# Kernel tuning notes

Measured on AMD Instinct MI355X. Metric: run time of the kernel, lower is better.

Reference implementation:

```python
import jax, jax.numpy as jnp
import numpy as np
from jax import lax

B, C_G, H, W = 2, 64, 240, 1216
NUM, K, IDX_REF = 8, 9, 4  # prop_kernel=3
PROP_TIME = 6


def conv3x3(x, w, b):
    y = lax.conv_general_dilated(x, w, (1, 1), ((1, 1), (1, 1)),
                                 dimension_numbers=('NCHW', 'OIHW', 'NCHW'))
    return y + b[None, :, None, None]


def bilinear_sample(img, y, x):
    """img: (B,H,W); y,x: (B,K,H,W) absolute coords; zero padding outside."""
    Hh, Ww = img.shape[1], img.shape[2]
    y0 = jnp.floor(y)
    x0 = jnp.floor(x)
    wy1, wx1 = y - y0, x - x0
    gather = jax.vmap(lambda im, a, b: im[a, b])
    out = jnp.zeros_like(y)
    for i, (yy, wy) in enumerate(((y0, 1.0 - wy1), (y0 + 1.0, wy1))):
        for j, (xx, wx) in enumerate(((x0, 1.0 - wx1), (x0 + 1.0, wx1))):
            valid = (yy >= 0) & (yy <= Hh - 1) & (xx >= 0) & (xx <= Ww - 1)
            yi = jnp.clip(yy, 0, Hh - 1).astype(jnp.int32)
            xi = jnp.clip(xx, 0, Ww - 1).astype(jnp.int32)
            v = gather(img, yi, xi)
            out = out + wy * wx * jnp.where(valid, v, 0.0)
    return out


def setup_inputs() -> dict:
    key = jax.random.key(0)
    ks = jax.random.split(key, 6)
    return {
        'initial_disp': jax.random.uniform(ks[0], (B, 1, H, W), jnp.float32) * 50.0,
        'occlus_mask': jax.random.uniform(ks[1], (B, 1, H, W), jnp.float32),
        'confidence': jax.random.uniform(ks[2], (B, 1, H, W), jnp.float32),
        'guidance_feature': jax.random.normal(ks[3], (B, C_G, H, W), jnp.float32),
        'conv_w': 0.05 * jax.random.normal(ks[4], (3 * NUM, C_G, 3, 3), jnp.float32),
        'conv_b': jnp.zeros((3 * NUM,), jnp.float32),
        'aff_scale_const': jnp.full((1,), 0.5 * NUM, jnp.float32),  # TGASS: gamma*num
    }


def nlspn_forward(initial_disp, occlus_mask, confidence, guidance_feature,
                  conv_w, conv_b, aff_scale_const):
    Bb, _, Hh, Ww = guidance_feature.shape
    oa = conv3x3(guidance_feature, conv_w, conv_b)          # (B, 3*num, H, W)
    o1, o2, aff = oa[:, :NUM], oa[:, NUM:2 * NUM], oa[:, 2 * NUM:]
    off = jnp.concatenate([o1, o2], axis=1).reshape(Bb, NUM, 2, Hh, Ww)
    zero = jnp.zeros((Bb, 1, 2, Hh, Ww), off.dtype)
    off = jnp.concatenate([off[:, :IDX_REF], zero, off[:, IDX_REF:]], axis=1)  # (B,9,2,H,W)

    # TGASS affinity
    aff = jnp.tanh(aff) / (aff_scale_const[0] + 1e-8)       # (B,8,H,W)

    gy = jnp.arange(Hh, dtype=jnp.float32)[None, None, :, None]
    gx = jnp.arange(Ww, dtype=jnp.float32)[None, None, None, :]

    # confidence sampling: 1x1 deform conv (w_conf=1, bias=0), detached offsets
    off_sg = lax.stop_gradient(off)
    nb = jnp.array([0, 1, 2, 3, 5, 6, 7, 8])
    conf_s = bilinear_sample(confidence[:, 0],
                             gy + off_sg[:, nb, 0], gx + off_sg[:, nb, 1])  # (B,8,H,W)
    aff = aff * conf_s

    s = jnp.sum(jnp.abs(aff), axis=1, keepdims=True) + 1e-5
    s = jnp.where(s < 1.0, 1.0, s)
    aff = aff / s
    aff_ref = 1.0 - jnp.sum(aff, axis=1, keepdims=True)
    aff_full = jnp.concatenate([aff[:, :IDX_REF], aff_ref, aff[:, IDX_REF:]], axis=1)  # (B,9,H,W)

    # 3x3 deform conv grid (stride 1, pad 1, dil 1), weight=ones, bias=0
    kh = (jnp.arange(K) // 3 - 1).astype(jnp.float32).reshape(1, K, 1, 1)
    kw = (jnp.arange(K) % 3 - 1).astype(jnp.float32).reshape(1, K, 1, 1)
    sy = gy + kh + off[:, :, 0]
    sx = gx + kw + off[:, :, 1]

    disp = initial_disp
    list_disp = []
    for _ in range(PROP_TIME):
        samp = bilinear_sample(disp[:, 0], sy, sx)           # (B,9,H,W)
        disp = jnp.sum(aff_full * samp, axis=1, keepdims=True)
        disp = jnp.maximum(disp, 0.0)
        disp = (1.0 - occlus_mask) * disp + occlus_mask * initial_disp
        list_disp.append(disp)
    disp = jnp.maximum(disp, 0.0)

    offset_flat = off.reshape(Bb, 2 * K, Hh, Ww)
    return disp, jnp.stack(list_disp), offset_flat, aff_full, aff_scale_const


def reference(initial_disp, occlus_mask, confidence, guidance_feature,
              conv_w, conv_b, aff_scale_const):
    return nlspn_forward(initial_disp, occlus_mask, confidence, guidance_feature,
                         conv_w, conv_b, aff_scale_const)
```

## Files before the change

kernel.cpp:

```cpp
#include <hip/hip_runtime.h>
#include <hip/hip_bf16.h>
#include <math.h>
#include <string.h>

typedef __attribute__((ext_vector_type(8))) short bf16x8;
typedef __attribute__((ext_vector_type(4))) float f32x4;

constexpr int Bc = 2, CGc = 64, Hc = 240, Wc = 1216;
constexpr int IDXR = 4, PROP = 6;
constexpr long HW  = (long)Hc * Wc;
constexpr long BHW = (long)Bc * HW;

constexpr long OUT0 = 0;
constexpr long OUT1 = BHW;
constexpr long OUT2 = BHW * 7;
constexpr long OUT3 = OUT2 + (long)Bc * 18 * HW;
constexpr long OUT4 = OUT3 + (long)Bc * 9 * HW;

constexpr int HP = Hc + 2, WPAD = Wc + 2;
constexpr long APXB   = (long)HP * WPAD;
constexpr long A_TOT  = (long)Bc * APXB * 128;
constexpr long WOFF   = A_TOT;
constexpr long WS_NEED = WOFF + (long)9 * 32 * 128;

constexpr int PR = 4, PC = 64, HLO = 6;
constexpr int TR = PR + 2 * HLO;
constexpr int TC = PC + 2 * HLO + 1;

__device__ __forceinline__ unsigned short f2bf(float f) {
  __hip_bfloat16 h = __float2bfloat16(f);
  return __builtin_bit_cast(unsigned short, h);
}

__device__ __forceinline__ void row2(const float* __restrict__ img, int yy, int x0,
                                     float& a, float& b) {
  if (yy >= 0 && yy < Hc) {
    if (x0 >= 0 && x0 < Wc - 1) {
      float2 v;
      __builtin_memcpy(&v, img + (long)yy * Wc + x0, 8);
      a = v.x; b = v.y;
    } else {
      a = (x0 >= 0 && x0 < Wc)         ? img[(long)yy * Wc + x0]     : 0.f;
      b = (x0 + 1 >= 0 && x0 + 1 < Wc) ? img[(long)yy * Wc + x0 + 1] : 0.f;
    }
  } else { a = 0.f; b = 0.f; }
}

__device__ __forceinline__ float bilin(const float* __restrict__ img, float y, float x) {
  float y0f = floorf(y), x0f = floorf(x);
  int y0 = (int)y0f, x0 = (int)x0f;
  float wy = y - y0f, wx = x - x0f;
  float v00, v01, v10, v11;
  row2(img, y0,     x0, v00, v01);
  row2(img, y0 + 1, x0, v10, v11);
  float top = v00 + wx * (v01 - v00);
  float bot = v10 + wx * (v11 - v10);
  return top + wy * (bot - top);
}

__device__ __forceinline__ float bilin_tile(
    const float (*tile)[TC], const float* __restrict__ db,
    int y0, int x0, float sy, float sx) {
  float yf = floorf(sy), xf = floorf(sx);
  int iy = (int)yf, ix = (int)xf;
  float wy = sy - yf, wx = sx - xf;
  if (iy >= y0 - HLO && iy + 1 <= y0 + PR - 1 + HLO &&
      ix >= x0 - HLO && ix + 1 <= x0 + PC - 1 + HLO) {
    int ly = iy - (y0 - HLO), lx = ix - (x0 - HLO);
    float v00 = tile[ly][lx],     v01 = tile[ly][lx + 1];
    float v10 = tile[ly + 1][lx], v11 = tile[ly + 1][lx + 1];
    float top = v00 + wx * (v01 - v00);
    float bot = v10 + wx * (v11 - v10);
    return top + wy * (bot - top);
  }
  return bilin(db, sy, sx);
}

__device__ __forceinline__ void stage_tile(
    float (*tile)[TC], const float* __restrict__ db, int y0, int x0, int tid) {
  for (int i = tid; i < TR * TC; i += 256) {
    int rr = i / TC, cc = i - rr * TC;
    int gy = y0 - HLO + rr, gx = x0 - HLO + cc;
    tile[rr][cc] = (gy >= 0 && gy < Hc && gx >= 0 && gx < Wc)
                       ? db[(long)gy * Wc + gx] : 0.f;
  }
}

__global__ __launch_bounds__(256) void nhwc_kernel(
    const float* __restrict__ g, char* __restrict__ ws) {
  __shared__ __align__(16) char tileb[64 * 132];
  const int tid = threadIdx.x;
  const int x0 = blockIdx.x * 64;
  const int y  = blockIdx.y;
  const int bz = blockIdx.z;
  const float* gb = g + (long)bz * CGc * HW + (long)y * Wc + x0;
  const int px = tid & 63, wv = tid >> 6;
#pragma unroll
  for (int k = 0; k < 16; ++k) {
    int ic = k * 4 + wv;
    float v = gb[(long)ic * HW + px];
    *reinterpret_cast<unsigned short*>(tileb + px * 132 + ic * 2) = f2bf(v);
  }
  __syncthreads();
  const int opx = tid >> 2, q = tid & 3;
  unsigned int u[8];
#pragma unroll
  for (int j = 0; j < 8; ++j)
    u[j] = *reinterpret_cast<unsigned int*>(tileb + opx * 132 + q * 32 + j * 4);
  char* dst = ws + ((long)(bz * HP + y + 1) * WPAD + x0 + 1 + opx) * 128 + q * 32;
  reinterpret_cast<uint4*>(dst)[0] = make_uint4(u[0], u[1], u[2], u[3]);
  reinterpret_cast<uint4*>(dst)[1] = make_uint4(u[4], u[5], u[6], u[7]);
}

__global__ __launch_bounds__(256) void border_kernel(char* __restrict__ ws) {
  constexpr int NB = 2 * WPAD + 2 * (HP - 2);
  long i = (long)blockIdx.x * 256 + threadIdx.x;
  if (i >= (long)Bc * NB) return;
  int bz = (int)(i / NB);
  int r  = (int)(i - (long)bz * NB);
  int py, px;
  if (r < WPAD)            { py = 0;      px = r; }
  else if (r < 2 * WPAD)   { py = HP - 1; px = r - WPAD; }
  else { int qq = r - 2 * WPAD; py = 1 + (qq >> 1); px = (qq & 1) ? (WPAD - 1) : 0; }
  char* p = ws + ((long)(bz * HP + py) * WPAD + px) * 128;
  uint4 z = make_uint4(0, 0, 0, 0);
#pragma unroll
  for (int j = 0; j < 8; ++j) reinterpret_cast<uint4*>(p)[j] = z;
}

__global__ __launch_bounds__(256) void wconv_kernel(
    const float* __restrict__ w, char* __restrict__ ws) {
  char* wd = ws + WOFF;
  int idx = blockIdx.x * 256 + threadIdx.x;
  if (idx < 24 * 64 * 9) {
    int oc = idx / 576, r = idx - oc * 576;
    int ic = r / 9, tap = r - ic * 9;
    *reinterpret_cast<unsigned short*>(wd + tap * 4096 + oc * 128 + ic * 2) = f2bf(w[idx]);
  } else if (idx < 32 * 64 * 9) {
    int i2 = idx - 24 * 64 * 9;
    int oc = 24 + i2 / 576, r = i2 % 576;
    int ic = r / 9, tap = r % 9;
    *reinterpret_cast<unsigned short*>(wd + tap * 4096 + oc * 128 + ic * 2) = 0;
  }
}

constexpr int CTILE_BYTES = 6 * 66 * 128;
constexpr int CUNITS = CTILE_BYTES / 16;

__global__ __launch_bounds__(256) void conv_lds_kernel(
    const char* __restrict__ ws, const float* __restrict__ bias,
    float* __restrict__ out) {
  __shared__ __align__(16) char smemA[CTILE_BYTES];
  const int tid  = threadIdx.x;
  const int lane = tid & 63, wv = tid >> 6;
  const int lrow = lane & 15, lgrp = lane >> 4;
  const int x0 = blockIdx.x * 64;
  const int y0 = blockIdx.y * 4;
  const int bz = blockIdx.z;

  const char* Abase = ws + ((long)(bz * HP + y0) * WPAD + x0) * 128;
#pragma unroll
  for (int it = 0; it < 13; ++it) {
    int u = it * 256 + tid;
    if (u < CUNITS) {
      int pxl = u >> 3, j = u & 7;
      int r = pxl / 66, col = pxl - r * 66;
      uint4 v = *reinterpret_cast<const uint4*>(
          Abase + ((long)r * WPAD + col) * 128 + j * 16);
      int ldsb = pxl * 128 + ((j ^ (col & 7)) << 4);
      *reinterpret_cast<uint4*>(smemA + ldsb) = v;
    }
  }
  __syncthreads();

  const char* Wb = ws + WOFF + (long)lrow * 128 + lgrp * 16;

  f32x4 acc[4][2];
#pragma unroll
  for (int h = 0; h < 4; ++h)
#pragma unroll
    for (int nt = 0; nt < 2; ++nt) acc[h][nt] = (f32x4){0.f, 0.f, 0.f, 0.f};

#pragma unroll
  for (int tap = 0; tap < 9; ++tap) {
    const int dy = tap / 3, dx = tap - dy * 3;
    const char* Wt = Wb + tap * 4096;
#pragma unroll
    for (int ks = 0; ks < 2; ++ks) {
      bf16x8 wf0 = *reinterpret_cast<const bf16x8*>(Wt + ks * 64);
      bf16x8 wf1 = *reinterpret_cast<const bf16x8*>(Wt + 2048 + ks * 64);
#pragma unroll
      for (int h = 0; h < 4; ++h) {
        const int colc = lrow + dx + h * 16;
        int abyte = ((wv + dy) * 66 + colc) * 128 +
                    ((((ks << 2) + lgrp) ^ (colc & 7)) << 4);
        bf16x8 af = *reinterpret_cast<const bf16x8*>(smemA + abyte);
        acc[h][0] = __builtin_amdgcn_mfma_f32_16x16x32_bf16(af, wf0, acc[h][0], 0, 0, 0);
        acc[h][1] = __builtin_amdgcn_mfma_f32_16x16x32_bf16(af, wf1, acc[h][1], 0, 0, 0);
      }
    }
  }

  const int y = y0 + wv;
#pragma unroll
  for (int h = 0; h < 4; ++h) {
    const int xx = x0 + h * 16 + lgrp * 4;
#pragma unroll
    for (int nt = 0; nt < 2; ++nt) {
      int oc = nt * 16 + lrow;
      if (oc >= 24) continue;
      float bv = bias[oc];
      long dst;
      if (oc < 16) {
        int n = oc >> 1, cd = oc & 1;
        int mm = (n < IDXR) ? n : n + 1;
        dst = OUT2 + (long)(bz * 18 + 2 * mm + cd) * HW;
      } else {
        int i2 = oc - 16;
        int mm = (i2 < IDXR) ? i2 : i2 + 1;
        dst = OUT3 + (long)(bz * 9 + mm) * HW;
      }
      f32x4 v = acc[h][nt];
      float4 st = make_float4(v[0] + bv, v[1] + bv, v[2] + bv, v[3] + bv);
      *reinterpret_cast<float4*>(&out[dst + (long)y * Wc + xx]) = st;
    }
  }
}

__global__ __launch_bounds__(256) void prep_prop0_kernel(
    const float* __restrict__ conf, const float* __restrict__ scale_p,
    const float* __restrict__ occm, const float* __restrict__ initd,
    float* __restrict__ out) {
  __shared__ float tile[TR][TC];
  const int tid = threadIdx.x;
  const int x0 = blockIdx.x * PC;
  const int y0 = blockIdx.y * PR;
  const int b  = blockIdx.z;
  const float* db = initd + (long)b * HW;
  stage_tile(tile, db, y0, x0, tid);
  __syncthreads();

  const int y = y0 + (tid >> 6);
  const int x = x0 + (tid & 63);
  long rem = (long)y * Wc + x;
  long p = (long)b * HW + rem;

  const float inv_scale = 1.f / (scale_p[0] + 1e-8f);
  const float* confb = conf + (long)b * HW;
  float* off  = out + OUT2 + (long)b * 18 * HW + rem;
  float* affp = out + OUT3 + (long)b * 9  * HW + rem;

  float affr[9], oyr[9], oxr[9];
  float asum = 0.f;
#pragma unroll
  for (int m = 0; m < 8; m++) {
    int n = (m < IDXR) ? m : m + 1;
    float oy  = off[(long)(2 * n) * HW];
    float ox  = off[(long)(2 * n + 1) * HW];
    float raw = affp[(long)n * HW];
    float avv = tanhf(raw) * inv_scale;
    float cs  = bilin(confb, (float)y + oy, (float)x + ox);
    affr[n] = avv * cs;
    oyr[n] = oy; oxr[n] = ox;
    asum += fabsf(affr[n]);
  }
  float s = fmaxf(asum + 1e-5f, 1.0f);
  float inv_s = 1.f / s;
  float total = 0.f;
#pragma unroll
  for (int m = 0; m < 8; m++) {
    int n = (m < IDXR) ? m : m + 1;
    affr[n] *= inv_s; total += affr[n];
  }
  affr[IDXR] = 1.f - total;
  oyr[IDXR] = 0.f; oxr[IDXR] = 0.f;
#pragma unroll
  for (int n = 0; n < 9; n++) affp[(long)n * HW] = affr[n];
  off[(long)(2 * IDXR) * HW]     = 0.f;
  off[(long)(2 * IDXR + 1) * HW] = 0.f;
  if (p == 0) out[OUT4] = scale_p[0];

  float acc = 0.f;
#pragma unroll
  for (int k = 0; k < 9; k++) {
    float sy = (float)(y + k / 3 - 1) + oyr[k];
    float sx = (float)(x + k % 3 - 1) + oxr[k];
    acc = fmaf(affr[k], bilin_tile(tile, db, y0, x0, sy, sx), acc);
  }
  acc = fmaxf(acc, 0.f);
  float o = occm[p];
  float res = (1.f - o) * acc + o * db[rem];
  out[OUT1 + p] = res;
}

__global__ __launch_bounds__(256) void prop_tile_kernel(
    const float* __restrict__ dispPrev,
    const float* __restrict__ occ, const float* __restrict__ initd,
    float* __restrict__ out, int t) {
  __shared__ float tile[TR][TC];
  const int tid = threadIdx.x;
  const int x0 = blockIdx.x * PC;
  const int y0 = blockIdx.y * PR;
  const int b  = blockIdx.z;
  const float* db = dispPrev + (long)b * HW;
  stage_tile(tile, db, y0, x0, tid);
  __syncthreads();

  const int y = y0 + (tid >> 6);
  const int x = x0 + (tid & 63);
  long rem = (long)y * Wc + x;
  long p = (long)b * HW + rem;

  const float* off  = out + OUT2 + (long)b * 18 * HW + rem;
  const float* affp = out + OUT3 + (long)b * 9  * HW + rem;

  float acc = 0.f;
#pragma unroll
  for (int k = 0; k < 9; k++) {
    float oy = off[(long)(2 * k) * HW];
    float ox = off[(long)(2 * k + 1) * HW];
    float av = affp[(long)k * HW];
    float sy = (float)(y + k / 3 - 1) + oy;
    float sx = (float)(x + k % 3 - 1) + ox;
    acc = fmaf(av, bilin_tile(tile, db, y0, x0, sy, sx), acc);
  }
  acc = fmaxf(acc, 0.f);
  float o = occ[p];
  float res = (1.f - o) * acc + o * initd[p];
  out[OUT1 + (long)t * BHW + p] = res;
  if (t == PROP - 1) out[OUT0 + p] = res;
}

constexpr int TY = 8, TX = 32;
constexpr int AR = TY + 2, AC = TX + 2;
constexpr int A_BYTES = AR * AC * CGc * 2;
constexpr int W_BYTES = 9 * 32 * 32 * 2;

__global__ __launch_bounds__(256) void conv_mfma_kernel(
    const float* __restrict__ g, const float* __restrict__ wsrc,
    const float* __restrict__ bias, float* __restrict__ out) {
  __shared__ __align__(16) char smemA[A_BYTES];
  __shared__ __align__(16) char smemW[W_BYTES];
  const int tid = threadIdx.x;
  const int x0 = blockIdx.x * TX;
  const int y0 = blockIdx.y * TY;
  const int bz = blockIdx.z;
  const float* gb = g + (long)bz * CGc * HW;
  for (int w = tid; w < AR * AC * 32; w += 256) {
    int c  = w % AC;
    int t2 = w / AC;
    int icp = t2 & 31;
    int r   = t2 >> 5;
    int y = y0 + r - 1, x = x0 + c - 1;
    float v0 = 0.f, v1 = 0.f;
    if (y >= 0 && y < Hc && x >= 0 && x < Wc) {
      const float* p = gb + (long)(2 * icp) * HW + (long)y * Wc + x;
      v0 = p[0]; v1 = p[HW];
    }
    unsigned int pk = (unsigned int)f2bf(v0) | ((unsigned int)f2bf(v1) << 16);
    int byte = (r * AC + c) * 128 + icp * 4;
    byte ^= (c & 7) << 4;
    *reinterpret_cast<unsigned int*>(smemA + byte) = pk;
  }
  auto stageW = [&](int hs) {
    for (int idx = tid; idx < 24 * 32 * 9; idx += 256) {
      int oc  = idx / 288;
      int r1  = idx - oc * 288;
      int icl = r1 / 9;
      int tap = r1 - icl * 9;
      float f = wsrc[idx + 288 * (oc + hs)];
      int byte = (tap * 32 + oc) * 64 + icl * 2;
      byte ^= (oc & 7) << 4;
      *reinterpret_cast<unsigned short*>(smemW + byte) = f2bf(f);
    }
  };
  stageW(0);
  __syncthreads();
  const int wid  = tid >> 6;
  const int lane = tid & 63;
  const int lrow = lane & 15;
  const int lgrp = lane >> 4;
  f32x4 acc[4][2];
#pragma unroll
  for (int m = 0; m < 4; m++)
#pragma unroll
    for (int nt = 0; nt < 2; nt++) acc[m][nt] = (f32x4){0.f, 0.f, 0.f, 0.f};
  for (int ks = 0; ks < 2; ++ks) {
    if (ks) { __syncthreads(); stageW(1); __syncthreads(); }
#pragma unroll
    for (int tap = 0; tap < 9; ++tap) {
      const int dy = tap / 3, dx = tap - dy * 3;
      int bb = (tap * 32 + lrow) * 64 + lgrp * 16;
      int bbyte0 = bb ^ ((lrow & 7) << 4);
      int bbyte1 = (bb + 16 * 64) ^ ((lrow & 7) << 4);
      bf16x8 bf0 = *reinterpret_cast<const bf16x8*>(smemW + bbyte0);
      bf16x8 bf1 = *reinterpret_cast<const bf16x8*>(smemW + bbyte1);
#pragma unroll
      for (int dr = 0; dr < 2; ++dr) {
        const int rin = 2 * wid + dr + dy;
#pragma unroll
        for (int h = 0; h < 2; ++h) {
          const int cin = h * 16 + lrow + dx;
          int abyte = ((rin * AC + cin) * 128 + ks * 64 + lgrp * 16) ^ ((cin & 7) << 4);
          bf16x8 af = *reinterpret_cast<const bf16x8*>(smemA + abyte);
          acc[dr * 2 + h][0] = __builtin_amdgcn_mfma_f32_16x16x32_bf16(af, bf0, acc[dr * 2 + h][0], 0, 0, 0);
          acc[dr * 2 + h][1] = __builtin_amdgcn_mfma_f32_16x16x32_bf16(af, bf1, acc[dr * 2 + h][1], 0, 0, 0);
        }
      }
    }
  }
#pragma unroll
  for (int dr = 0; dr < 2; ++dr) {
    const int yy = y0 + 2 * wid + dr;
#pragma unroll
    for (int h = 0; h < 2; ++h) {
      const int xx = x0 + h * 16 + lgrp * 4;
#pragma unroll
      for (int nt = 0; nt < 2; ++nt) {
        int oc = nt * 16 + lrow;
        if (oc >= 24) continue;
        float bv = bias[oc];
        long dst;
        if (oc < 16) {
          int n = oc >> 1, cd = oc & 1;
          int mm = (n < IDXR) ? n : n + 1;
          dst = OUT2 + (long)(bz * 18 + 2 * mm + cd) * HW;
        } else {
          int i2 = oc - 16;
          int mm = (i2 < IDXR) ? i2 : i2 + 1;
          dst = OUT3 + (long)(bz * 9 + mm) * HW;
        }
        f32x4 v = acc[dr * 2 + h][nt];
        float4 st = make_float4(v[0] + bv, v[1] + bv, v[2] + bv, v[3] + bv);
        *reinterpret_cast<float4*>(&out[dst + (long)yy * Wc + xx]) = st;
      }
    }
  }
}

__global__ __launch_bounds__(256) void prep_kernel(
    const float* __restrict__ conf, const float* __restrict__ scale_p,
    float* __restrict__ out) {
  long p = (long)blockIdx.x * 256 + threadIdx.x;
  if (p >= BHW) return;
  int b = (int)(p / HW);
  long rem = p - (long)b * HW;
  int y = (int)(rem / Wc);
  int x = (int)(rem - (long)y * Wc);
  const float inv_scale = 1.f / (scale_p[0] + 1e-8f);
  const float* confb = conf + (long)b * HW;
  float* off  = out + OUT2 + (long)b * 18 * HW + rem;
  float* affp = out + OUT3 + (long)b * 9  * HW + rem;
  float a[8];
  float asum = 0.f;
#pragma unroll
  for (int m = 0; m < 8; m++) {
    int n = (m < IDXR) ? m : m + 1;
    float oy  = off[(long)(2 * n) * HW];
    float ox  = off[(long)(2 * n + 1) * HW];
    float raw = affp[(long)n * HW];
    float av  = tanhf(raw) * inv_scale;
    float cs  = bilin(confb, (float)y + oy, (float)x + ox);
    a[m] = av * cs;
    asum += fabsf(a[m]);
  }
  float s = fmaxf(asum + 1e-5f, 1.0f);
  float inv_s = 1.f / s;
  float total = 0.f;
#pragma unroll
  for (int m = 0; m < 8; m++) { a[m] *= inv_s; total += a[m]; }
  float aref = 1.f - total;
#pragma unroll
  for (int m = 0; m < 8; m++) {
    int n = (m < IDXR) ? m : m + 1;
    affp[(long)n * HW] = a[m];
  }
  affp[(long)IDXR * HW] = aref;
  off[(long)(2 * IDXR) * HW]     = 0.f;
  off[(long)(2 * IDXR + 1) * HW] = 0.f;
  if (p == 0) out[OUT4] = scale_p[0];
}

__global__ __launch_bounds__(256) void prop_kernel(
    const float* __restrict__ dispPrev,
    const float* __restrict__ occ, const float* __restrict__ initd,
    float* __restrict__ out, int t) {
  long p = (long)blockIdx.x * 256 + threadIdx.x;
  if (p >= BHW) return;
  int b = (int)(p / HW);
  long rem = p - (long)b * HW;
  int y = (int)(rem / Wc);
  int x = (int)(rem - (long)y * Wc);
  const float* off  = out + OUT2 + (long)b * 18 * HW + rem;
  const float* affp = out + OUT3 + (long)b * 9  * HW + rem;
  const float* db   = dispPrev + (long)b * HW;
  float acc = 0.f;
#pragma unroll
  for (int k = 0; k < 9; k++) {
    float oy = off[(long)(2 * k) * HW];
    float ox = off[(long)(2 * k + 1) * HW];
    float av = affp[(long)k * HW];
    float sy = (float)(y + k / 3 - 1) + oy;
    float sx = (float)(x + k % 3 - 1) + ox;
    acc = fmaf(av, bilin(db, sy, sx), acc);
  }
  acc = fmaxf(acc, 0.f);
  float o = occ[p];
  float res = (1.f - o) * acc + o * initd[p];
  out[OUT1 + (long)t * BHW + p] = res;
  if (t == PROP - 1) out[OUT0 + p] = res;
}

extern "C" void kernel_launch(void* const* d_in, const int* in_sizes, int n_in,
                              void* d_out, int out_size, void* d_ws, size_t ws_size,
                              hipStream_t stream) {
  const float* initd = (const float*)d_in[0];
  const float* occ   = (const float*)d_in[1];
  const float* conf  = (const float*)d_in[2];
  const float* guid  = (const float*)d_in[3];
  const float* cw    = (const float*)d_in[4];
  const float* cb    = (const float*)d_in[5];
  const float* csc   = (const float*)d_in[6];
  float* out = (float*)d_out;
  int nblk = (int)((BHW + 255) / 256);

  if (ws_size >= (size_t)WS_NEED) {
    char* ws = (char*)d_ws;
    nhwc_kernel<<<dim3(Wc / 64, Hc, Bc), 256, 0, stream>>>(guid, ws);
    border_kernel<<<(Bc * (2 * WPAD + 2 * (HP - 2)) + 255) / 256, 256, 0, stream>>>(ws);
    wconv_kernel<<<72, 256, 0, stream>>>(cw, ws);
    conv_lds_kernel<<<dim3(Wc / 64, Hc / 4, Bc), 256, 0, stream>>>(ws, cb, out);

    dim3 pgrid(Wc / PC, Hc / PR, Bc);
    prep_prop0_kernel<<<pgrid, 256, 0, stream>>>(conf, csc, occ, initd, out);
    for (int t = 1; t < PROP; t++) {
      const float* dp = out + OUT1 + (long)(t - 1) * BHW;
      prop_tile_kernel<<<pgrid, 256, 0, stream>>>(dp, occ, initd, out, t);
    }
  } else {
    conv_mfma_kernel<<<dim3(Wc / TX, Hc / TY, Bc), 256, 0, stream>>>(guid, cw, cb, out);
    prep_kernel<<<nblk, 256, 0, stream>>>(conf, csc, out);
    for (int t = 0; t < PROP; t++) {
      const float* dp = (t == 0) ? initd : (out + OUT1 + (long)(t - 1) * BHW);
      prop_kernel<<<nblk, 256, 0, stream>>>(dp, occ, initd, out, t);
    }
  }
}
```

Measured before the change: 240.7 us.

## Pack per-pixel propagation params into float4 table and stage confidence in LDS

The prep kernel now writes a packed per-pixel table (9 affinities, 9+9 offsets, occlusion and initial disparity) as eight float4 planes in the workspace. The later propagation kernels read this table with vector loads instead of 29 scalar strided loads from the output planes. The confidence map is also staged into a shared-memory tile for bilinear sampling. The workspace already holds the NHWC conv data, so reusing it after the conv is assumed safe. The cost is an extra 128 B per pixel written once, and the per-step read volume grows slightly because of padding.

After: 241.6 us. Within noise of the previous version (+0.4%).

```diff
diff --git a/kernel.cpp b/kernel.cpp
--- a/kernel.cpp
+++ b/kernel.cpp
@@ -230,14 +230,17 @@
 __global__ __launch_bounds__(256) void prep_prop0_kernel(
     const float* __restrict__ conf, const float* __restrict__ scale_p,
     const float* __restrict__ occm, const float* __restrict__ initd,
-    float* __restrict__ out) {
+    float* __restrict__ out, float4* __restrict__ tab4) {
   __shared__ float tile[TR][TC];
+  __shared__ float ctile[TR][TC];
   const int tid = threadIdx.x;
   const int x0 = blockIdx.x * PC;
   const int y0 = blockIdx.y * PR;
   const int b  = blockIdx.z;
-  const float* db = initd + (long)b * HW;
-  stage_tile(tile, db, y0, x0, tid);
+  const float* db    = initd + (long)b * HW;
+  const float* confb = conf  + (long)b * HW;
+  stage_tile(tile,  db,    y0, x0, tid);
+  stage_tile(ctile, confb, y0, x0, tid);
   __syncthreads();
 
   const int y = y0 + (tid >> 6);
@@ -246,7 +249,6 @@
   long p = (long)b * HW + rem;
 
   const float inv_scale = 1.f / (scale_p[0] + 1e-8f);
-  const float* confb = conf + (long)b * HW;
   float* off  = out + OUT2 + (long)b * 18 * HW + rem;
   float* affp = out + OUT3 + (long)b * 9  * HW + rem;
 
@@ -259,7 +261,7 @@
     float ox  = off[(long)(2 * n + 1) * HW];
     float raw = affp[(long)n * HW];
     float avv = tanhf(raw) * inv_scale;
-    float cs  = bilin(confb, (float)y + oy, (float)x + ox);
+    float cs  = bilin_tile(ctile, confb, y0, x0, (float)y + oy, (float)x + ox);
     affr[n] = avv * cs;
     oyr[n] = oy; oxr[n] = ox;
     asum += fabsf(affr[n]);
@@ -280,6 +282,8 @@
   off[(long)(2 * IDXR + 1) * HW] = 0.f;
   if (p == 0) out[OUT4] = scale_p[0];
 
+  float occv  = occm[p];
+  float initv = db[rem];
   float acc = 0.f;
 #pragma unroll
   for (int k = 0; k < 9; k++) {
@@ -288,14 +292,20 @@
     acc = fmaf(affr[k], bilin_tile(tile, db, y0, x0, sy, sx), acc);
   }
   acc = fmaxf(acc, 0.f);
-  float o = occm[p];
-  float res = (1.f - o) * acc + o * db[rem];
+  float res = (1.f - occv) * acc + occv * initv;
   out[OUT1 + p] = res;
-}
-
-__global__ __launch_bounds__(256) void prop_tile_kernel(
-    const float* __restrict__ dispPrev,
-    const float* __restrict__ occ, const float* __restrict__ initd,
+
+  float fl[32];
+#pragma unroll
+  for (int k = 0; k < 9; k++) { fl[k] = affr[k]; fl[9 + k] = oyr[k]; fl[18 + k] = oxr[k]; }
+  fl[27] = occv; fl[28] = initv; fl[29] = 0.f; fl[30] = 0.f; fl[31] = 0.f;
+#pragma unroll
+  for (int g = 0; g < 8; g++)
+    tab4[(long)g * BHW + p] = make_float4(fl[4 * g], fl[4 * g + 1], fl[4 * g + 2], fl[4 * g + 3]);
+}
+
+__global__ __launch_bounds__(256) void prop_tab_kernel(
+    const float* __restrict__ dispPrev, const float4* __restrict__ tab4,
     float* __restrict__ out, int t) {
   __shared__ float tile[TR][TC];
   const int tid = threadIdx.x;
@@ -311,22 +321,22 @@
   long rem = (long)y * Wc + x;
   long p = (long)b * HW + rem;
 
-  const float* off  = out + OUT2 + (long)b * 18 * HW + rem;
-  const float* affp = out + OUT3 + (long)b * 9  * HW + rem;
+  float fl[32];
+#pragma unroll
+  for (int g = 0; g < 8; g++) {
+    float4 v = tab4[(long)g * BHW + p];
+    fl[4 * g] = v.x; fl[4 * g + 1] = v.y; fl[4 * g + 2] = v.z; fl[4 * g + 3] = v.w;
+  }
 
   float acc = 0.f;
 #pragma unroll
   for (int k = 0; k < 9; k++) {
-    float oy = off[(long)(2 * k) * HW];
-    float ox = off[(long)(2 * k + 1) * HW];
-    float av = affp[(long)k * HW];
-    float sy = (float)(y + k / 3 - 1) + oy;
-    float sx = (float)(x + k % 3 - 1) + ox;
-    acc = fmaf(av, bilin_tile(tile, db, y0, x0, sy, sx), acc);
+    float sy = (float)(y + k / 3 - 1) + fl[9 + k];
+    float sx = (float)(x + k % 3 - 1) + fl[18 + k];
+    acc = fmaf(fl[k], bilin_tile(tile, db, y0, x0, sy, sx), acc);
   }
   acc = fmaxf(acc, 0.f);
-  float o = occ[p];
-  float res = (1.f - o) * acc + o * initd[p];
+  float res = (1.f - fl[27]) * acc + fl[27] * fl[28];
   out[OUT1 + (long)t * BHW + p] = res;
   if (t == PROP - 1) out[OUT0 + p] = res;
 }
@@ -531,11 +541,12 @@
     wconv_kernel<<<72, 256, 0, stream>>>(cw, ws);
     conv_lds_kernel<<<dim3(Wc / 64, Hc / 4, Bc), 256, 0, stream>>>(ws, cb, out);
 
+    float4* tab4 = (float4*)ws;
     dim3 pgrid(Wc / PC, Hc / PR, Bc);
-    prep_prop0_kernel<<<pgrid, 256, 0, stream>>>(conf, csc, occ, initd, out);
+    prep_prop0_kernel<<<pgrid, 256, 0, stream>>>(conf, csc, occ, initd, out, tab4);
     for (int t = 1; t < PROP; t++) {
       const float* dp = out + OUT1 + (long)(t - 1) * BHW;
-      prop_tile_kernel<<<pgrid, 256, 0, stream>>>(dp, occ, initd, out, t);
+      prop_tab_kernel<<<pgrid, 256, 0, stream>>>(dp, tab4, out, t);
     }
   } else {
     conv_mfma_kernel<<<dim3(Wc / TX, Hc / TY, Bc), 256, 0, stream>>>(guid, cw, cb, out);
```

## Fuse conv epilogue with affinity prep and first propagation step

Applied to the files above, without the earlier changes.

Merges the conv MFMA kernel with the prep/prop0 kernel. Conv outputs go through an LDS exchange buffer, so the fused kernel no longer re-reads offsets and affinity logits from global memory. The confidence map is also staged in LDS for the bilinear sampling, and the affinity output no longer takes a separate raw write followed by a read. The fused kernel relies on the prop grid (PC/PR) matching the conv tiling of 64x4, and LDS reuse of the conv tile buffer must fit within CTILE_BYTES.

New measurement: 223.3 us. 7.2% less time.

```diff
diff --git a/kernel.cpp b/kernel.cpp
--- a/kernel.cpp
+++ b/kernel.cpp
@@ -146,9 +146,14 @@
 
 constexpr int CTILE_BYTES = 6 * 66 * 128;
 constexpr int CUNITS = CTILE_BYTES / 16;
-
-__global__ __launch_bounds__(256) void conv_lds_kernel(
+constexpr int EXCH_BYTES = 4 * 64 * 25 * 4;
+constexpr int DT_OFF = EXCH_BYTES;
+constexpr int CT_OFF = DT_OFF + TR * TC * 4;
+
+__global__ __launch_bounds__(256) void conv_fused_kernel(
     const char* __restrict__ ws, const float* __restrict__ bias,
+    const float* __restrict__ conf, const float* __restrict__ scale_p,
+    const float* __restrict__ occm, const float* __restrict__ initd,
     float* __restrict__ out) {
   __shared__ __align__(16) char smemA[CTILE_BYTES];
   const int tid  = threadIdx.x;
@@ -200,66 +205,67 @@
       }
     }
   }
-
-  const int y = y0 + wv;
-#pragma unroll
-  for (int h = 0; h < 4; ++h) {
-    const int xx = x0 + h * 16 + lgrp * 4;
-#pragma unroll
-    for (int nt = 0; nt < 2; ++nt) {
-      int oc = nt * 16 + lrow;
-      if (oc >= 24) continue;
-      float bv = bias[oc];
-      long dst;
-      if (oc < 16) {
-        int n = oc >> 1, cd = oc & 1;
-        int mm = (n < IDXR) ? n : n + 1;
-        dst = OUT2 + (long)(bz * 18 + 2 * mm + cd) * HW;
-      } else {
-        int i2 = oc - 16;
-        int mm = (i2 < IDXR) ? i2 : i2 + 1;
-        dst = OUT3 + (long)(bz * 9 + mm) * HW;
+  __syncthreads();
+
+  float* exch = reinterpret_cast<float*>(smemA);
+  {
+    const int y = y0 + wv;
+#pragma unroll
+    for (int h = 0; h < 4; ++h) {
+      const int xx = x0 + h * 16 + lgrp * 4;
+      const int lpx = h * 16 + lgrp * 4;
+#pragma unroll
+      for (int nt = 0; nt < 2; ++nt) {
+        int oc = nt * 16 + lrow;
+        if (oc >= 24) continue;
+        float bv = bias[oc];
+        f32x4 v = acc[h][nt];
+#pragma unroll
+        for (int j = 0; j < 4; ++j)
+          exch[(wv * 64 + lpx + j) * 25 + oc] = v[j] + bv;
+        if (oc < 16) {
+          int n = oc >> 1, cd = oc & 1;
+          int mm = (n < IDXR) ? n : n + 1;
+          long dst = OUT2 + (long)(bz * 18 + 2 * mm + cd) * HW;
+          float4 st = make_float4(v[0] + bv, v[1] + bv, v[2] + bv, v[3] + bv);
+          *reinterpret_cast<float4*>(&out[dst + (long)y * Wc + xx]) = st;
+        }
       }
-      f32x4 v = acc[h][nt];
-      float4 st = make_float4(v[0] + bv, v[1] + bv, v[2] + bv, v[3] + bv);
-      *reinterpret_cast<float4*>(&out[dst + (long)y * Wc + xx]) = st;
-    }
-  }
-}
-
-__global__ __launch_bounds__(256) void prep_prop0_kernel(
-    const float* __restrict__ conf, const float* __restrict__ scale_p,
-    const float* __restrict__ occm, const float* __restrict__ initd,
-    float* __restrict__ out) {
-  __shared__ float tile[TR][TC];
-  const int tid = threadIdx.x;
-  const int x0 = blockIdx.x * PC;
-  const int y0 = blockIdx.y * PR;
-  const int b  = blockIdx.z;
-  const float* db = initd + (long)b * HW;
-  stage_tile(tile, db, y0, x0, tid);
-  __syncthreads();
-
-  const int y = y0 + (tid >> 6);
-  const int x = x0 + (tid & 63);
+    }
+  }
+  __syncthreads();
+
+  float (*dtile)[TC] = reinterpret_cast<float (*)[TC]>(smemA + DT_OFF);
+  float (*ctile)[TC] = reinterpret_cast<float (*)[TC]>(smemA + CT_OFF);
+  const float* db    = initd + (long)bz * HW;
+  const float* confb = conf  + (long)bz * HW;
+  stage_tile(dtile, db,    y0, x0, tid);
+  stage_tile(ctile, confb, y0, x0, tid);
+  __syncthreads();
+
+  const int row = tid >> 6, px = tid & 63;
+  const int y = y0 + row, x = x0 + px;
   long rem = (long)y * Wc + x;
-  long p = (long)b * HW + rem;
+  long p = (long)bz * HW + rem;
+
+  float ch[24];
+#pragma unroll
+  for (int j = 0; j < 24; ++j) ch[j] = exch[(row * 64 + px) * 25 + j];
 
   const float inv_scale = 1.f / (scale_p[0] + 1e-8f);
-  const float* confb = conf + (long)b * HW;
-  float* off  = out + OUT2 + (long)b * 18 * HW + rem;
-  float* affp = out + OUT3 + (long)b * 9  * HW + rem;
+  float* off  = out + OUT2 + (long)bz * 18 * HW + rem;
+  float* affp = out + OUT3 + (long)bz * 9  * HW + rem;
 
   float affr[9], oyr[9], oxr[9];
   float asum = 0.f;
 #pragma unroll
   for (int m = 0; m < 8; m++) {
     int n = (m < IDXR) ? m : m + 1;
-    float oy  = off[(long)(2 * n) * HW];
-    float ox  = off[(long)(2 * n + 1) * HW];
-    float raw = affp[(long)n * HW];
+    float oy  = ch[2 * m];
+    float ox  = ch[2 * m + 1];
+    float raw = ch[16 + m];
     float avv = tanhf(raw) * inv_scale;
-    float cs  = bilin(confb, (float)y + oy, (float)x + ox);
+    float cs  = bilin_tile(ctile, confb, y0, x0, (float)y + oy, (float)x + ox);
     affr[n] = avv * cs;
     oyr[n] = oy; oxr[n] = ox;
     asum += fabsf(affr[n]);
@@ -280,17 +286,17 @@
   off[(long)(2 * IDXR + 1) * HW] = 0.f;
   if (p == 0) out[OUT4] = scale_p[0];
 
-  float acc = 0.f;
+  float occv  = occm[p];
+  float initv = db[rem];
+  float acc0 = 0.f;
 #pragma unroll
   for (int k = 0; k < 9; k++) {
     float sy = (float)(y + k / 3 - 1) + oyr[k];
     float sx = (float)(x + k % 3 - 1) + oxr[k];
-    acc = fmaf(affr[k], bilin_tile(tile, db, y0, x0, sy, sx), acc);
-  }
-  acc = fmaxf(acc, 0.f);
-  float o = occm[p];
-  float res = (1.f - o) * acc + o * db[rem];
-  out[OUT1 + p] = res;
+    acc0 = fmaf(affr[k], bilin_tile(dtile, db, y0, x0, sy, sx), acc0);
+  }
+  acc0 = fmaxf(acc0, 0.f);
+  out[OUT1 + p] = (1.f - occv) * acc0 + occv * initv;
 }
 
 __global__ __launch_bounds__(256) void prop_tile_kernel(
@@ -529,10 +535,9 @@
     nhwc_kernel<<<dim3(Wc / 64, Hc, Bc), 256, 0, stream>>>(guid, ws);
     border_kernel<<<(Bc * (2 * WPAD + 2 * (HP - 2)) + 255) / 256, 256, 0, stream>>>(ws);
     wconv_kernel<<<72, 256, 0, stream>>>(cw, ws);
-    conv_lds_kernel<<<dim3(Wc / 64, Hc / 4, Bc), 256, 0, stream>>>(ws, cb, out);
 
     dim3 pgrid(Wc / PC, Hc / PR, Bc);
-    prep_prop0_kernel<<<pgrid, 256, 0, stream>>>(conf, csc, occ, initd, out);
+    conv_fused_kernel<<<pgrid, 256, 0, stream>>>(ws, cb, conf, csc, occ, initd, out);
     for (int t = 1; t < PROP; t++) {
       const float* dp = out + OUT1 + (long)(t - 1) * BHW;
       prop_tile_kernel<<<pgrid, 256, 0, stream>>>(dp, occ, initd, out, t);
```
